# Performance work log

Hardware: AMD Instinct MI355X
Metric: run time of the kernel (lower is better)

The kernel has to match this reference:

```python
import jax, jax.numpy as jnp
import numpy as np

N = 30000       # nodes
E = 480000      # edges (before self-loops)
G = 64          # graphs in batch
IN = 128        # in_channels
HID = 128       # hidden_dim
HEADS = 4
NEG_SLOPE = 0.2


def gat_layer(x, src, dst, W, att_src, att_dst, b):
    """PyG-style GATConv: W [Fin, H*C], att_* [H, C], b [H*C]. Returns [N, H*C] (head concat)."""
    H, C = att_src.shape
    h = (x @ W).reshape(-1, H, C)                      # [N, H, C]
    a_s = jnp.einsum('nhc,hc->nh', h, att_src)         # [N, H]
    a_d = jnp.einsum('nhc,hc->nh', h, att_dst)
    e = jax.nn.leaky_relu(a_s[src] + a_d[dst], NEG_SLOPE)   # [Etot, H]
    # segment softmax over edges grouped by destination node
    m = jax.ops.segment_max(e, dst, num_segments=N)
    e = jnp.exp(e - m[dst])
    denom = jax.ops.segment_sum(e, dst, num_segments=N)
    alpha = e / (denom[dst] + 1e-16)                   # [Etot, H]
    msg = h[src] * alpha[:, :, None]                   # [Etot, H, C]
    out = jax.ops.segment_sum(msg, dst, num_segments=N)
    return out.reshape(-1, H * C) + b


def setup_inputs():
    key = jax.random.key(0)
    ks = jax.random.split(key, 13)
    s = 0.05
    x = jax.random.normal(ks[0], (N, IN), jnp.float32)
    edge_index = jax.random.randint(ks[1], (2, E), 0, N, dtype=jnp.int32)
    batch = jnp.sort(jax.random.randint(ks[2], (N,), 0, G, dtype=jnp.int32))
    return {
        'x': x,
        'edge_index': edge_index,
        'batch': batch,
        'W1': jax.random.normal(ks[3], (IN, HEADS * HID), jnp.float32) * s,
        'att_src1': jax.random.normal(ks[4], (HEADS, HID), jnp.float32) * s,
        'att_dst1': jax.random.normal(ks[5], (HEADS, HID), jnp.float32) * s,
        'b1': jnp.zeros((HEADS * HID,), jnp.float32),
        'W2': jax.random.normal(ks[6], (HEADS * HID, HID), jnp.float32) * s,
        'att_src2': jax.random.normal(ks[7], (1, HID), jnp.float32) * s,
        'att_dst2': jax.random.normal(ks[8], (1, HID), jnp.float32) * s,
        'b2': jnp.zeros((HID,), jnp.float32),
        'lin_w': jax.random.normal(ks[9], (HID, 1), jnp.float32) * s,
        'lin_b': jnp.zeros((1,), jnp.float32),
    }


def reference(x, edge_index, batch, W1, att_src1, att_dst1, b1, W2, att_src2, att_dst2, b2, lin_w, lin_b):
    # add self-loops (PyG GATConv default)
    loop = jnp.arange(N, dtype=edge_index.dtype)
    src = jnp.concatenate([edge_index[0], loop])
    dst = jnp.concatenate([edge_index[1], loop])

    h = gat_layer(x, src, dst, W1, att_src1, att_dst1, b1)   # [N, 4*HID]
    h = jax.nn.elu(h)
    h = gat_layer(h, src, dst, W2, att_src2, att_dst2, b2)   # [N, HID]
    h = jax.nn.elu(h)

    # global mean pool over graphs
    sums = jax.ops.segment_sum(h, batch, num_segments=G)     # [G, HID]
    cnts = jax.ops.segment_sum(jnp.ones((N,), h.dtype), batch, num_segments=G)
    pooled = sums / jnp.maximum(cnts, 1.0)[:, None]

    out = pooled @ lin_w + lin_b                             # [G, 1]
    return out.squeeze(-1)                                   # [G]
```

## Files before the change

### kernel.cpp

```cpp
#include <hip/hip_runtime.h>

#define NN    30000
#define EE    480000
#define ETOT  (EE + NN)
#define GG    64
#define IN_CH 128
#define HID   128
#define HEADS 4
#define F1    (HEADS * HID)
#define CAP   64

typedef __attribute__((ext_vector_type(8))) __bf16 bf16x8;
typedef __attribute__((ext_vector_type(4))) float  floatx4;
typedef __attribute__((ext_vector_type(2))) float  f32x2;

__device__ __forceinline__ float lrelu(float x) { return x > 0.f ? x : 0.2f * x; }
__device__ __forceinline__ float elu_f(float x) { return x > 0.f ? x : (expf(x) - 1.f); }
__device__ __forceinline__ unsigned short f2bf(float f) {
    unsigned int u = __float_as_uint(f);
    return (unsigned short)((u + 0x7FFFu + ((u >> 16) & 1u)) >> 16);
}
__device__ __forceinline__ float bf2f(unsigned short u) {
    return __uint_as_float(((unsigned int)u) << 16);
}
__device__ __forceinline__ f32x2 fma2(float a, f32x2 v, f32x2 acc) {
    f32x2 av = {a, a};
    return __builtin_elementwise_fma(av, v, acc);
}

#define LDKC 136
__global__ __launch_bounds__(256) void gemm_bf16(const unsigned short* __restrict__ A, int lda, int zA,
                                                 const unsigned short* __restrict__ Bt, int zBt, int K,
                                                 unsigned short* __restrict__ C, int ldc, int zC,
                                                 const float* __restrict__ bias, int zBias,
                                                 int M, int do_elu,
                                                 const float* __restrict__ ws,
                                                 const float* __restrict__ wd,
                                                 float* __restrict__ as_out,
                                                 float* __restrict__ ad_out)
{
    A  += (size_t)blockIdx.z * zA;
    Bt += (size_t)blockIdx.z * zBt;
    C  += (size_t)blockIdx.z * zC;
    const float* bias_p = bias ? bias + (size_t)blockIdx.z * zBias : nullptr;

    __shared__ unsigned short Bl[128 * LDKC];

    const int tid  = threadIdx.x;
    const int wave = tid >> 6, lane = tid & 63;
    const int quad = lane >> 4, l16 = lane & 15;
    const int bm = blockIdx.x * 128;

    floatx4 zf = {0.f, 0.f, 0.f, 0.f};
    floatx4 acc[2][8];
#pragma unroll
    for (int rt = 0; rt < 2; rt++)
#pragma unroll
        for (int ct = 0; ct < 8; ct++) acc[rt][ct] = zf;

    float bb[8];
#pragma unroll
    for (int ct = 0; ct < 8; ct++) bb[ct] = bias_p ? bias_p[ct * 16 + l16] : 0.f;

    const int r0 = bm + wave * 32 + l16;
    const int r1 = r0 + 16;

    for (int kc = 0; kc < K; kc += 128) {
        uint4 av[2][4];
#pragma unroll
        for (int kb = 0; kb < 4; kb++) {
            const int k = kc + kb * 32 + quad * 8;
            av[0][kb] = (r0 < M) ? *(const uint4*)(A + (size_t)r0 * lda + k) : uint4{0,0,0,0};
            av[1][kb] = (r1 < M) ? *(const uint4*)(A + (size_t)r1 * lda + k) : uint4{0,0,0,0};
        }

        if (kc) __syncthreads();
#pragma unroll
        for (int i = 0; i < 8; i++) {
            int j = i * 256 + tid;
            int n = j >> 4, ko = (j & 15) * 8;
            *(uint4*)&Bl[n * LDKC + ko] = *(const uint4*)(Bt + (size_t)n * K + kc + ko);
        }
        __syncthreads();

#pragma unroll
        for (int kb = 0; kb < 4; kb++) {
            bf16x8 bfr[8];
#pragma unroll
            for (int ct = 0; ct < 8; ct++)
                bfr[ct] = *(bf16x8*)&Bl[(ct * 16 + l16) * LDKC + kb * 32 + quad * 8];
            bf16x8 a0 = *(bf16x8*)&av[0][kb];
            bf16x8 a1 = *(bf16x8*)&av[1][kb];
#pragma unroll
            for (int ct = 0; ct < 8; ct++) {
                acc[0][ct] = __builtin_amdgcn_mfma_f32_16x16x32_bf16(a0, bfr[ct], acc[0][ct], 0, 0, 0);
                acc[1][ct] = __builtin_amdgcn_mfma_f32_16x16x32_bf16(a1, bfr[ct], acc[1][ct], 0, 0, 0);
            }
        }
    }

    __syncthreads();
    unsigned short* wls = Bl + wave * (16 * 128);
#pragma unroll
    for (int rt = 0; rt < 2; rt++) {
        if (rt) __builtin_amdgcn_wave_barrier();
#pragma unroll
        for (int ct = 0; ct < 8; ct++) {
#pragma unroll
            for (int reg = 0; reg < 4; reg++) {
                float v = acc[rt][ct][reg] + bb[ct];
                if (do_elu) v = elu_f(v);
                wls[(quad * 4 + reg) * 128 + ct * 16 + l16] = f2bf(v);
            }
        }
        __builtin_amdgcn_wave_barrier();
#pragma unroll
        for (int i = 0; i < 4; i++) {
            int j = i * 64 + lane;
            int rl = j >> 4, off = (j & 15) * 8;
            int row = bm + wave * 32 + rt * 16 + rl;
            if (row < M)
                *(uint4*)(C + (size_t)row * ldc + off) = *(uint4*)&wls[rl * 128 + off];
        }
        if (ws) {
            int row = bm + wave * 32 + rt * 16 + l16;
            const unsigned short* rowp = &wls[l16 * 128 + quad * 32];
            float ps = 0.f, pd = 0.f;
#pragma unroll
            for (int jj = 0; jj < 32; jj++) {
                float hv = bf2f(rowp[jj]);
                ps = fmaf(hv, ws[quad * 32 + jj], ps);
                pd = fmaf(hv, wd[quad * 32 + jj], pd);
            }
            ps += __shfl_xor(ps, 16); ps += __shfl_xor(ps, 32);
            pd += __shfl_xor(pd, 16); pd += __shfl_xor(pd, 32);
            if (quad == 0 && row < M) { as_out[row] = ps; ad_out[row] = pd; }
        }
    }
}

__global__ void prep_k(const float* __restrict__ W1, const float* __restrict__ W2,
                       const float* __restrict__ att_s, const float* __restrict__ att_d,
                       unsigned short* __restrict__ W1t, unsigned short* __restrict__ W2t,
                       float* __restrict__ wt, int* __restrict__ deg,
                       float* __restrict__ pooled_cnt)
{
    int b = blockIdx.x;
    if (b < 256) {
        int idx = b * 256 + threadIdx.x;
        int h = idx >> 14, rem = idx & 16383, n = rem >> 7, k = rem & 127;
        W1t[idx] = f2bf(W1[(size_t)k * F1 + h * 128 + n]);
    } else if (b < 512) {
        int idx = (b - 256) * 256 + threadIdx.x;
        int n = idx >> 9, k = idx & 511;
        W2t[idx] = f2bf(W2[(size_t)k * HID + n]);
    } else if (b < 520) {
        if (threadIdx.x < 128) {
            int q = b - 512;
            int h = q & 3, sd = q >> 2;
            int i = threadIdx.x;
            const float* att = (sd ? att_d : att_s) + h * 128;
            const float* wr = W1 + (size_t)i * F1 + h * 128;
            float acc = 0.f;
            for (int c = 0; c < 128; c++) acc = fmaf(wr[c], att[c], acc);
            wt[sd * 512 + h * 128 + i] = acc;
        }
    } else if (b < 638) {
        int i = (b - 520) * 256 + threadIdx.x;
        if (i < NN) deg[i] = 0;
    } else {
        int i = (b - 638) * 256 + threadIdx.x;
        if (i < GG * HID + GG) pooled_cnt[i] = 0.f;
    }
}

__global__ __launch_bounds__(128) void score1_k(const float* __restrict__ x,
                                                const float* __restrict__ wt,
                                                float* __restrict__ a_s,
                                                float* __restrict__ a_d,
                                                unsigned short* __restrict__ x16)
{
    __shared__ __align__(16) float swt[1024];
    int t = threadIdx.x;
    ((float4*)swt)[t]       = ((const float4*)wt)[t];
    ((float4*)swt)[t + 128] = ((const float4*)wt)[t + 128];
    __syncthreads();
    const int node0 = blockIdx.x * 16;
    int node = node0 + (t >> 3);
    int q = t & 7;
    int h = q & 3, sd = q >> 2;
    if (node < NN) {
        const float4* xr = (const float4*)(x + (size_t)node * IN_CH);
        const float4* wr = (const float4*)(swt + sd * 512 + h * 128);
        float acc = 0.f;
#pragma unroll 4
        for (int c = 0; c < 32; c++) {
            float4 xv = xr[c], wv = wr[c];
            acc = fmaf(xv.x, wv.x, acc);
            acc = fmaf(xv.y, wv.y, acc);
            acc = fmaf(xv.z, wv.z, acc);
            acc = fmaf(xv.w, wv.w, acc);
        }
        if (sd == 0) a_s[node * 4 + h] = acc;
        else         a_d[node * 4 + h] = acc;
    }
#pragma unroll 4
    for (int r = 0; r < 16; r++) {
        int nr = node0 + r;
        if (nr < NN)
            x16[(size_t)nr * IN_CH + t] = f2bf(x[(size_t)nr * IN_CH + t]);
    }
}

__global__ void fill_k(const int* __restrict__ ei, int* __restrict__ deg, int* __restrict__ perm)
{
    int i = blockIdx.x * blockDim.x + threadIdx.x;
    if (i < ETOT) {
        int s, d;
        if (i < EE) { s = ei[i]; d = ei[EE + i]; }
        else        { s = i - EE; d = i - EE; }
        int p = atomicAdd(&deg[d], 1);
        if (p < CAP) perm[(size_t)d * CAP + p] = s;
    }
}

__global__ __launch_bounds__(256) void gat_agg1w(const unsigned short* __restrict__ x16,
                                                 const float* __restrict__ a_s,
                                                 const float* __restrict__ a_d,
                                                 const int* __restrict__ deg,
                                                 const int* __restrict__ perm,
                                                 unsigned short* __restrict__ agg)
{
    __shared__ int    sSrc[4][64];
    __shared__ __align__(16) float4 sE[4][64];
    const int wave = threadIdx.x >> 6;
    const int lane = threadIdx.x & 63;
    int n = blockIdx.x * 4 + wave;
    if (n >= NN) return;
    const int rem = min(deg[n], CAP);
    const float4 ad4 = *(const float4*)(a_d + (size_t)n * 4);

    f32x2 acc0 = {0.f, 0.f}, acc1 = {0.f, 0.f}, acc2 = {0.f, 0.f}, acc3 = {0.f, 0.f};
    f32x2 den01 = {0.f, 0.f}, den23 = {0.f, 0.f};

    if (lane < rem) {
        int sj = perm[(size_t)n * CAP + lane];
        float4 av = *(const float4*)(a_s + (size_t)sj * 4);
        sSrc[wave][lane] = sj;
        sE[wave][lane] = make_float4(__expf(lrelu(av.x + ad4.x)), __expf(lrelu(av.y + ad4.y)),
                                     __expf(lrelu(av.z + ad4.z)), __expf(lrelu(av.w + ad4.w)));
    }
    __builtin_amdgcn_wave_barrier();
    for (int j = 0; j < rem; j++) {
        int s = sSrc[wave][j];
        float4 ev = sE[wave][j];
        den01 += (f32x2){ev.x, ev.y};
        den23 += (f32x2){ev.z, ev.w};
        unsigned int uv = *(const unsigned int*)(x16 + (size_t)s * IN_CH + lane * 2);
        f32x2 xv = { __uint_as_float(uv << 16), __uint_as_float(uv & 0xFFFF0000u) };
        acc0 = fma2(ev.x, xv, acc0);
        acc1 = fma2(ev.y, xv, acc1);
        acc2 = fma2(ev.z, xv, acc2);
        acc3 = fma2(ev.w, xv, acc3);
    }
    const float i0 = 1.f / (den01.x + 1e-16f), i1 = 1.f / (den01.y + 1e-16f);
    const float i2 = 1.f / (den23.x + 1e-16f), i3 = 1.f / (den23.y + 1e-16f);

    unsigned short* ag = agg + (size_t)n * F1 + lane * 2;
    *(unsigned int*)(ag + 0 * 128) = (unsigned)f2bf(acc0.x * i0) | ((unsigned)f2bf(acc0.y * i0) << 16);
    *(unsigned int*)(ag + 1 * 128) = (unsigned)f2bf(acc1.x * i1) | ((unsigned)f2bf(acc1.y * i1) << 16);
    *(unsigned int*)(ag + 2 * 128) = (unsigned)f2bf(acc2.x * i2) | ((unsigned)f2bf(acc2.y * i2) << 16);
    *(unsigned int*)(ag + 3 * 128) = (unsigned)f2bf(acc3.x * i3) | ((unsigned)f2bf(acc3.y * i3) << 16);
}

__global__ __launch_bounds__(256) void gat_agg2w(const unsigned short* __restrict__ h16,
                                                 const float* __restrict__ a_s,
                                                 const float* __restrict__ a_d,
                                                 const int* __restrict__ deg,
                                                 const int* __restrict__ perm,
                                                 const float* __restrict__ bias,
                                                 unsigned short* __restrict__ out16)
{
    int n = blockIdx.x * 4 + (threadIdx.x >> 6);
    if (n >= NN) return;
    const int lane = threadIdx.x & 63;
    const int rem = min(deg[n], CAP);
    const float ad = a_d[n];

    f32x2 acc = {0.f, 0.f};
    float den = 0.f;
    int sj = 0;
    float e = 0.f;
    if (lane < rem) {
        sj = perm[(size_t)n * CAP + lane];
        e = __expf(lrelu(a_s[sj] + ad));
    }
    for (int j = 0; j < rem; j++) {
        int   s = __shfl(sj, j);
        float a = __shfl(e, j);
        den += a;
        unsigned int uv = *(const unsigned int*)(h16 + (size_t)s * HID + lane * 2);
        f32x2 hv = { __uint_as_float(uv << 16), __uint_as_float(uv & 0xFFFF0000u) };
        acc = fma2(a, hv, acc);
    }
    const float inv = 1.f / (den + 1e-16f);
    float2 bb = *(const float2*)(bias + lane * 2);
    float v0 = elu_f(acc.x * inv + bb.x);
    float v1 = elu_f(acc.y * inv + bb.y);
    *(unsigned int*)(out16 + (size_t)n * HID + lane * 2) =
        (unsigned)f2bf(v0) | ((unsigned)f2bf(v1) << 16);
}

#define NPB 64
__global__ __launch_bounds__(128) void pool_seg_k(const unsigned short* __restrict__ out16,
                                                  const int* __restrict__ batch,
                                                  float* __restrict__ pooled,
                                                  float* __restrict__ cnt)
{
    int n0 = blockIdx.x * NPB;
    int n1 = min(n0 + NPB, NN);
    if (n0 >= n1) return;
    int t = threadIdx.x;
    int cur = batch[n0];
    float acc = 0.f;
    int count = 0;
    for (int n = n0; n < n1; n++) {
        int g = batch[n];
        if (g != cur) {
            atomicAdd(&pooled[cur * HID + t], acc);
            if (t == 0) atomicAdd(&cnt[cur], (float)count);
            acc = 0.f; count = 0; cur = g;
        }
        acc += bf2f(out16[(size_t)n * HID + t]);
        count++;
    }
    atomicAdd(&pooled[cur * HID + t], acc);
    if (t == 0) atomicAdd(&cnt[cur], (float)count);
}

__global__ void final_k(const float* __restrict__ pooled, const float* __restrict__ cnt,
                        const float* __restrict__ lw, const float* __restrict__ lb,
                        float* __restrict__ outp)
{
    int g = threadIdx.x;
    if (g < GG) {
        float acc = 0.f;
        for (int c = 0; c < HID; c++) acc += pooled[g * HID + c] * lw[c];
        float cc = fmaxf(cnt[g], 1.0f);
        outp[g] = acc / cc + lb[0];
    }
}

extern "C" void kernel_launch(void* const* d_in, const int* in_sizes, int n_in,
                              void* d_out, int out_size, void* d_ws, size_t ws_size,
                              hipStream_t stream)
{
    const float* x    = (const float*)d_in[0];
    const int*   ei   = (const int*)d_in[1];
    const int*   batch= (const int*)d_in[2];
    const float* W1   = (const float*)d_in[3];
    const float* as1w = (const float*)d_in[4];
    const float* ad1w = (const float*)d_in[5];
    const float* b1   = (const float*)d_in[6];
    const float* W2   = (const float*)d_in[7];
    const float* as2w = (const float*)d_in[8];
    const float* ad2w = (const float*)d_in[9];
    const float* b2   = (const float*)d_in[10];
    const float* lw   = (const float*)d_in[11];
    const float* lb   = (const float*)d_in[12];
    float* outp = (float*)d_out;

    char* w = (char*)d_ws;
    size_t off = 0;
    auto alloc = [&](size_t bytes) -> char* {
        char* p = w + off;
        off += (bytes + 255) & ~(size_t)255;
        return p;
    };
    char*  reg0   = alloc((size_t)NN * F1 * 4);
    char*  reg1   = alloc((size_t)NN * F1 * 2);
    unsigned short* x16 = (unsigned short*)alloc((size_t)NN * IN_CH * 2);
    unsigned short* W1t = (unsigned short*)alloc(65536 * 2);
    unsigned short* W2t = (unsigned short*)alloc(65536 * 2);
    float* wt1    = (float*)alloc(1024 * 4);
    float* a_s1   = (float*)alloc((size_t)NN * 4 * 4);
    float* a_d1   = (float*)alloc((size_t)NN * 4 * 4);
    float* a_s2   = (float*)alloc((size_t)NN * 4);
    float* a_d2   = (float*)alloc((size_t)NN * 4);
    int*   deg    = (int*)alloc((size_t)NN * 4);
    int*   perm   = (int*)alloc((size_t)NN * CAP * 4);
    float* pooled = (float*)alloc((size_t)(GG * HID + GG) * 4);
    float* cnt    = pooled + GG * HID;

    unsigned short* agg16   = (unsigned short*)reg0;
    unsigned short* out116  = (unsigned short*)reg1;
    unsigned short* hh2_16  = (unsigned short*)reg0;
    unsigned short* out2_16 = (unsigned short*)reg0 + (size_t)NN * HID;

    prep_k<<<671, 256, 0, stream>>>(W1, W2, as1w, ad1w, W1t, W2t, wt1, deg, pooled);
    score1_k<<<(NN + 15) / 16, 128, 0, stream>>>(x, wt1, a_s1, a_d1, x16);
    fill_k<<<(ETOT + 255) / 256, 256, 0, stream>>>(ei, deg, perm);

    gat_agg1w<<<(NN + 3) / 4, 256, 0, stream>>>(x16, a_s1, a_d1, deg, perm, agg16);
    const int MT = (NN + 127) / 128;
    gemm_bf16<<<dim3(MT, 1, 4), 256, 0, stream>>>(agg16, F1, 128, W1t, 128 * 128, 128,
                                                  out116, F1, 128, b1, 128, NN, 1,
                                                  nullptr, nullptr, nullptr, nullptr);

    gemm_bf16<<<dim3(MT, 1, 1), 256, 0, stream>>>(out116, F1, 0, W2t, 0, F1,
                                                  hh2_16, HID, 0, nullptr, 0, NN, 0,
                                                  as2w, ad2w, a_s2, a_d2);
    gat_agg2w<<<(NN + 3) / 4, 256, 0, stream>>>(hh2_16, a_s2, a_d2, deg, perm, b2, out2_16);

    pool_seg_k<<<(NN + NPB - 1) / NPB, 128, 0, stream>>>(out2_16, batch, pooled, cnt);
    final_k<<<1, 64, 0, stream>>>(pooled, cnt, lw, lb, outp);
}
```

Baseline: 249.8 us.

## Merge score/fill kernels, fold final into pool, split edges across half-waves

Score1 and fill run as one launch by splitting the grid by block index, and the final linear layer runs in the last pool block, found with an atomic done counter and a threadfence. This removes two kernel launches. Both aggregation kernels now split each node's edge list between the two half-waves, with each lane loading 8 bytes (4 bf16) per row, and combine the halves with a cross-half shuffle. This widens memory accesses and halves the serial edge loop, at the cost of extra shuffles and half the lanes idling on the layer-2 store.

New measurement: 265.8 us. 1.06x slower.

```diff
diff --git a/kernel.cpp b/kernel.cpp
--- a/kernel.cpp
+++ b/kernel.cpp
@@ -143,7 +143,7 @@
                        const float* __restrict__ att_s, const float* __restrict__ att_d,
                        unsigned short* __restrict__ W1t, unsigned short* __restrict__ W2t,
                        float* __restrict__ wt, int* __restrict__ deg,
-                       float* __restrict__ pooled_cnt)
+                       float* __restrict__ pooled_cnt_done)
 {
     int b = blockIdx.x;
     if (b < 256) {
@@ -170,57 +170,61 @@
         if (i < NN) deg[i] = 0;
     } else {
         int i = (b - 638) * 256 + threadIdx.x;
-        if (i < GG * HID + GG) pooled_cnt[i] = 0.f;
-    }
-}
-
-__global__ __launch_bounds__(128) void score1_k(const float* __restrict__ x,
-                                                const float* __restrict__ wt,
-                                                float* __restrict__ a_s,
-                                                float* __restrict__ a_d,
-                                                unsigned short* __restrict__ x16)
-{
-    __shared__ __align__(16) float swt[1024];
+        if (i < GG * HID + GG + 1) pooled_cnt_done[i] = 0.f;
+    }
+}
+
+#define SCORE_BLKS ((NN + 31) / 32)
+__global__ __launch_bounds__(256) void scorefill_k(const float* __restrict__ x,
+                                                   const float* __restrict__ wt,
+                                                   float* __restrict__ a_s,
+                                                   float* __restrict__ a_d,
+                                                   unsigned short* __restrict__ x16,
+                                                   const int* __restrict__ ei,
+                                                   int* __restrict__ deg,
+                                                   int* __restrict__ perm)
+{
+    int b = blockIdx.x;
     int t = threadIdx.x;
-    ((float4*)swt)[t]       = ((const float4*)wt)[t];
-    ((float4*)swt)[t + 128] = ((const float4*)wt)[t + 128];
-    __syncthreads();
-    const int node0 = blockIdx.x * 16;
-    int node = node0 + (t >> 3);
-    int q = t & 7;
-    int h = q & 3, sd = q >> 2;
-    if (node < NN) {
-        const float4* xr = (const float4*)(x + (size_t)node * IN_CH);
-        const float4* wr = (const float4*)(swt + sd * 512 + h * 128);
-        float acc = 0.f;
+    if (b < SCORE_BLKS) {
+        __shared__ __align__(16) float swt[1024];
+        ((float4*)swt)[t] = ((const float4*)wt)[t];
+        __syncthreads();
+        const int node0 = b * 32;
+        int node = node0 + (t >> 3);
+        int q = t & 7;
+        int h = q & 3, sd = q >> 2;
+        if (node < NN) {
+            const float4* xr = (const float4*)(x + (size_t)node * IN_CH);
+            const float4* wr = (const float4*)(swt + sd * 512 + h * 128);
+            float acc = 0.f;
 #pragma unroll 4
-        for (int c = 0; c < 32; c++) {
-            float4 xv = xr[c], wv = wr[c];
-            acc = fmaf(xv.x, wv.x, acc);
-            acc = fmaf(xv.y, wv.y, acc);
-            acc = fmaf(xv.z, wv.z, acc);
-            acc = fmaf(xv.w, wv.w, acc);
-        }
-        if (sd == 0) a_s[node * 4 + h] = acc;
-        else         a_d[node * 4 + h] = acc;
-    }
+            for (int c = 0; c < 32; c++) {
+                float4 xv = xr[c], wv = wr[c];
+                acc = fmaf(xv.x, wv.x, acc);
+                acc = fmaf(xv.y, wv.y, acc);
+                acc = fmaf(xv.z, wv.z, acc);
+                acc = fmaf(xv.w, wv.w, acc);
+            }
+            if (sd == 0) a_s[node * 4 + h] = acc;
+            else         a_d[node * 4 + h] = acc;
+        }
+        int col = t & 127;
 #pragma unroll 4
-    for (int r = 0; r < 16; r++) {
-        int nr = node0 + r;
-        if (nr < NN)
-            x16[(size_t)nr * IN_CH + t] = f2bf(x[(size_t)nr * IN_CH + t]);
-    }
-}
-
-__global__ void fill_k(const int* __restrict__ ei, int* __restrict__ deg, int* __restrict__ perm)
-{
-    int i = blockIdx.x * blockDim.x + threadIdx.x;
-    if (i < ETOT) {
-        int s, d;
-        if (i < EE) { s = ei[i]; d = ei[EE + i]; }
-        else        { s = i - EE; d = i - EE; }
-        int p = atomicAdd(&deg[d], 1);
-        if (p < CAP) perm[(size_t)d * CAP + p] = s;
+        for (int r = (t >> 7); r < 32; r += 2) {
+            int nr = node0 + r;
+            if (nr < NN)
+                x16[(size_t)nr * IN_CH + col] = f2bf(x[(size_t)nr * IN_CH + col]);
+        }
+    } else {
+        int i = (b - SCORE_BLKS) * 256 + t;
+        if (i < ETOT) {
+            int s, d;
+            if (i < EE) { s = ei[i]; d = ei[EE + i]; }
+            else        { s = i - EE; d = i - EE; }
+            int p = atomicAdd(&deg[d], 1);
+            if (p < CAP) perm[(size_t)d * CAP + p] = s;
+        }
     }
 }
 
@@ -235,13 +239,12 @@
     __shared__ __align__(16) float4 sE[4][64];
     const int wave = threadIdx.x >> 6;
     const int lane = threadIdx.x & 63;
+    const int hw   = lane >> 5;
+    const int c4   = (lane & 31) * 4;
     int n = blockIdx.x * 4 + wave;
     if (n >= NN) return;
     const int rem = min(deg[n], CAP);
     const float4 ad4 = *(const float4*)(a_d + (size_t)n * 4);
-
-    f32x2 acc0 = {0.f, 0.f}, acc1 = {0.f, 0.f}, acc2 = {0.f, 0.f}, acc3 = {0.f, 0.f};
-    f32x2 den01 = {0.f, 0.f}, den23 = {0.f, 0.f};
 
     if (lane < rem) {
         int sj = perm[(size_t)n * CAP + lane];
@@ -251,26 +254,45 @@
                                      __expf(lrelu(av.z + ad4.z)), __expf(lrelu(av.w + ad4.w)));
     }
     __builtin_amdgcn_wave_barrier();
-    for (int j = 0; j < rem; j++) {
+
+    f32x2 aLo[4] = {{0,0},{0,0},{0,0},{0,0}};
+    f32x2 aHi[4] = {{0,0},{0,0},{0,0},{0,0}};
+    f32x2 den01 = {0,0}, den23 = {0,0};
+
+    for (int j = hw; j < rem; j += 2) {
         int s = sSrc[wave][j];
         float4 ev = sE[wave][j];
         den01 += (f32x2){ev.x, ev.y};
         den23 += (f32x2){ev.z, ev.w};
-        unsigned int uv = *(const unsigned int*)(x16 + (size_t)s * IN_CH + lane * 2);
-        f32x2 xv = { __uint_as_float(uv << 16), __uint_as_float(uv & 0xFFFF0000u) };
-        acc0 = fma2(ev.x, xv, acc0);
-        acc1 = fma2(ev.y, xv, acc1);
-        acc2 = fma2(ev.z, xv, acc2);
-        acc3 = fma2(ev.w, xv, acc3);
-    }
-    const float i0 = 1.f / (den01.x + 1e-16f), i1 = 1.f / (den01.y + 1e-16f);
-    const float i2 = 1.f / (den23.x + 1e-16f), i3 = 1.f / (den23.y + 1e-16f);
-
-    unsigned short* ag = agg + (size_t)n * F1 + lane * 2;
-    *(unsigned int*)(ag + 0 * 128) = (unsigned)f2bf(acc0.x * i0) | ((unsigned)f2bf(acc0.y * i0) << 16);
-    *(unsigned int*)(ag + 1 * 128) = (unsigned)f2bf(acc1.x * i1) | ((unsigned)f2bf(acc1.y * i1) << 16);
-    *(unsigned int*)(ag + 2 * 128) = (unsigned)f2bf(acc2.x * i2) | ((unsigned)f2bf(acc2.y * i2) << 16);
-    *(unsigned int*)(ag + 3 * 128) = (unsigned)f2bf(acc3.x * i3) | ((unsigned)f2bf(acc3.y * i3) << 16);
+        uint2 uv = *(const uint2*)(x16 + (size_t)s * IN_CH + c4);
+        f32x2 xlo = { __uint_as_float(uv.x << 16), __uint_as_float(uv.x & 0xFFFF0000u) };
+        f32x2 xhi = { __uint_as_float(uv.y << 16), __uint_as_float(uv.y & 0xFFFF0000u) };
+        aLo[0] = fma2(ev.x, xlo, aLo[0]); aHi[0] = fma2(ev.x, xhi, aHi[0]);
+        aLo[1] = fma2(ev.y, xlo, aLo[1]); aHi[1] = fma2(ev.y, xhi, aHi[1]);
+        aLo[2] = fma2(ev.z, xlo, aLo[2]); aHi[2] = fma2(ev.z, xhi, aHi[2]);
+        aLo[3] = fma2(ev.w, xlo, aLo[3]); aHi[3] = fma2(ev.w, xhi, aHi[3]);
+    }
+#pragma unroll
+    for (int h = 0; h < 4; h++) {
+        aLo[h].x += __shfl_xor(aLo[h].x, 32); aLo[h].y += __shfl_xor(aLo[h].y, 32);
+        aHi[h].x += __shfl_xor(aHi[h].x, 32); aHi[h].y += __shfl_xor(aHi[h].y, 32);
+    }
+    den01.x += __shfl_xor(den01.x, 32); den01.y += __shfl_xor(den01.y, 32);
+    den23.x += __shfl_xor(den23.x, 32); den23.y += __shfl_xor(den23.y, 32);
+    const float iv0 = 1.f / (den01.x + 1e-16f), iv1 = 1.f / (den01.y + 1e-16f);
+    const float iv2 = 1.f / (den23.x + 1e-16f), iv3 = 1.f / (den23.y + 1e-16f);
+
+#pragma unroll
+    for (int k = 0; k < 2; k++) {
+        int h = hw * 2 + k;
+        f32x2 lo = hw ? aLo[2 + k] : aLo[k];
+        f32x2 hi = hw ? aHi[2 + k] : aHi[k];
+        float iv = hw ? (k ? iv3 : iv2) : (k ? iv1 : iv0);
+        uint2 o;
+        o.x = (unsigned)f2bf(lo.x * iv) | ((unsigned)f2bf(lo.y * iv) << 16);
+        o.y = (unsigned)f2bf(hi.x * iv) | ((unsigned)f2bf(hi.y * iv) << 16);
+        *(uint2*)(agg + (size_t)n * F1 + h * 128 + c4) = o;
+    }
 }
 
 __global__ __launch_bounds__(256) void gat_agg2w(const unsigned short* __restrict__ h16,
@@ -284,70 +306,85 @@
     int n = blockIdx.x * 4 + (threadIdx.x >> 6);
     if (n >= NN) return;
     const int lane = threadIdx.x & 63;
+    const int hw   = lane >> 5;
+    const int c4   = (lane & 31) * 4;
     const int rem = min(deg[n], CAP);
     const float ad = a_d[n];
 
-    f32x2 acc = {0.f, 0.f};
-    float den = 0.f;
-    int sj = 0;
-    float e = 0.f;
+    int sj = 0; float e = 0.f;
     if (lane < rem) {
         sj = perm[(size_t)n * CAP + lane];
         e = __expf(lrelu(a_s[sj] + ad));
     }
-    for (int j = 0; j < rem; j++) {
+    f32x2 accLo = {0,0}, accHi = {0,0};
+    float den = 0.f;
+    for (int j = hw; j < rem; j += 2) {
         int   s = __shfl(sj, j);
         float a = __shfl(e, j);
         den += a;
-        unsigned int uv = *(const unsigned int*)(h16 + (size_t)s * HID + lane * 2);
-        f32x2 hv = { __uint_as_float(uv << 16), __uint_as_float(uv & 0xFFFF0000u) };
-        acc = fma2(a, hv, acc);
-    }
+        uint2 uv = *(const uint2*)(h16 + (size_t)s * HID + c4);
+        f32x2 lo = { __uint_as_float(uv.x << 16), __uint_as_float(uv.x & 0xFFFF0000u) };
+        f32x2 hi = { __uint_as_float(uv.y << 16), __uint_as_float(uv.y & 0xFFFF0000u) };
+        accLo = fma2(a, lo, accLo);
+        accHi = fma2(a, hi, accHi);
+    }
+    accLo.x += __shfl_xor(accLo.x, 32); accLo.y += __shfl_xor(accLo.y, 32);
+    accHi.x += __shfl_xor(accHi.x, 32); accHi.y += __shfl_xor(accHi.y, 32);
+    den += __shfl_xor(den, 32);
     const float inv = 1.f / (den + 1e-16f);
-    float2 bb = *(const float2*)(bias + lane * 2);
-    float v0 = elu_f(acc.x * inv + bb.x);
-    float v1 = elu_f(acc.y * inv + bb.y);
-    *(unsigned int*)(out16 + (size_t)n * HID + lane * 2) =
-        (unsigned)f2bf(v0) | ((unsigned)f2bf(v1) << 16);
+    if (hw == 0) {
+        float4 bb = *(const float4*)(bias + c4);
+        uint2 o;
+        o.x = (unsigned)f2bf(elu_f(accLo.x * inv + bb.x)) |
+              ((unsigned)f2bf(elu_f(accLo.y * inv + bb.y)) << 16);
+        o.y = (unsigned)f2bf(elu_f(accHi.x * inv + bb.z)) |
+              ((unsigned)f2bf(elu_f(accHi.y * inv + bb.w)) << 16);
+        *(uint2*)(out16 + (size_t)n * HID + c4) = o;
+    }
 }
 
 #define NPB 64
 __global__ __launch_bounds__(128) void pool_seg_k(const unsigned short* __restrict__ out16,
                                                   const int* __restrict__ batch,
                                                   float* __restrict__ pooled,
-                                                  float* __restrict__ cnt)
+                                                  float* __restrict__ cnt,
+                                                  int* __restrict__ done,
+                                                  const float* __restrict__ lw,
+                                                  const float* __restrict__ lb,
+                                                  float* __restrict__ outp,
+                                                  int nblocks)
 {
     int n0 = blockIdx.x * NPB;
     int n1 = min(n0 + NPB, NN);
-    if (n0 >= n1) return;
     int t = threadIdx.x;
-    int cur = batch[n0];
-    float acc = 0.f;
-    int count = 0;
-    for (int n = n0; n < n1; n++) {
-        int g = batch[n];
-        if (g != cur) {
-            atomicAdd(&pooled[cur * HID + t], acc);
-            if (t == 0) atomicAdd(&cnt[cur], (float)count);
-            acc = 0.f; count = 0; cur = g;
-        }
-        acc += bf2f(out16[(size_t)n * HID + t]);
-        count++;
-    }
-    atomicAdd(&pooled[cur * HID + t], acc);
-    if (t == 0) atomicAdd(&cnt[cur], (float)count);
-}
-
-__global__ void final_k(const float* __restrict__ pooled, const float* __restrict__ cnt,
-                        const float* __restrict__ lw, const float* __restrict__ lb,
-                        float* __restrict__ outp)
-{
-    int g = threadIdx.x;
-    if (g < GG) {
+    if (n0 < n1) {
+        int cur = batch[n0];
         float acc = 0.f;
-        for (int c = 0; c < HID; c++) acc += pooled[g * HID + c] * lw[c];
-        float cc = fmaxf(cnt[g], 1.0f);
-        outp[g] = acc / cc + lb[0];
+        int count = 0;
+        for (int n = n0; n < n1; n++) {
+            int g = batch[n];
+            if (g != cur) {
+                atomicAdd(&pooled[cur * HID + t], acc);
+                if (t == 0) atomicAdd(&cnt[cur], (float)count);
+                acc = 0.f; count = 0; cur = g;
+            }
+            acc += bf2f(out16[(size_t)n * HID + t]);
+            count++;
+        }
+        atomicAdd(&pooled[cur * HID + t], acc);
+        if (t == 0) atomicAdd(&cnt[cur], (float)count);
+    }
+    __threadfence();
+    __shared__ int sLast;
+    if (t == 0) sLast = (atomicAdd(done, 1) == nblocks - 1);
+    __syncthreads();
+    if (sLast && t < GG) {
+        volatile const float* vp = pooled;
+        volatile const float* vc = cnt;
+        float acc = 0.f;
+        for (int c = 0; c < HID; c++) acc += vp[t * HID + c] * lw[c];
+        float cc = fmaxf(vc[t], 1.0f);
+        outp[t] = acc / cc + lb[0];
     }
 }
 
@@ -389,8 +426,9 @@
     float* a_d2   = (float*)alloc((size_t)NN * 4);
     int*   deg    = (int*)alloc((size_t)NN * 4);
     int*   perm   = (int*)alloc((size_t)NN * CAP * 4);
-    float* pooled = (float*)alloc((size_t)(GG * HID + GG) * 4);
+    float* pooled = (float*)alloc((size_t)(GG * HID + GG + 1) * 4);
     float* cnt    = pooled + GG * HID;
+    int*   done   = (int*)(pooled + GG * HID + GG);
 
     unsigned short* agg16   = (unsigned short*)reg0;
     unsigned short* out116  = (unsigned short*)reg1;
@@ -398,8 +436,10 @@
     unsigned short* out2_16 = (unsigned short*)reg0 + (size_t)NN * HID;
 
     prep_k<<<671, 256, 0, stream>>>(W1, W2, as1w, ad1w, W1t, W2t, wt1, deg, pooled);
-    score1_k<<<(NN + 15) / 16, 128, 0, stream>>>(x, wt1, a_s1, a_d1, x16);
-    fill_k<<<(ETOT + 255) / 256, 256, 0, stream>>>(ei, deg, perm);
+
+    const int FILL_BLKS = (ETOT + 255) / 256;
+    scorefill_k<<<SCORE_BLKS + FILL_BLKS, 256, 0, stream>>>(x, wt1, a_s1, a_d1, x16,
+                                                            ei, deg, perm);
 
     gat_agg1w<<<(NN + 3) / 4, 256, 0, stream>>>(x16, a_s1, a_d1, deg, perm, agg16);
     const int MT = (NN + 127) / 128;
@@ -412,6 +452,6 @@
                                                   as2w, ad2w, a_s2, a_d2);
     gat_agg2w<<<(NN + 3) / 4, 256, 0, stream>>>(hh2_16, a_s2, a_d2, deg, perm, b2, out2_16);
 
-    pool_seg_k<<<(NN + NPB - 1) / NPB, 128, 0, stream>>>(out2_16, batch, pooled, cnt);
-    final_k<<<1, 64, 0, stream>>>(pooled, cnt, lw, lb, outp);
-}
+    const int PB = (NN + NPB - 1) / NPB;
+    pool_seg_k<<<PB, 128, 0, stream>>>(out2_16, batch, pooled, cnt, done, lw, lb, outp, PB);
+}
```
